# Performance work log

Measured on AMD Instinct MI355X. Metric: run time of the kernel, lower is better.

The kernel has to match this reference:

```python
import jax, jax.numpy as jnp
import numpy as np

N, F, H, E = 100000, 128, 128, 3200000
EPS = 1e-5


def setup_inputs() -> dict:
    key = jax.random.key(0)
    ks = jax.random.split(key, 16)
    g = lambda k, shape, fan_in: jax.random.normal(k, shape, jnp.float32) / np.sqrt(fan_in)
    inp = {
        'x': jax.random.normal(ks[0], (N, F), jnp.float32),
        'edge_index': jax.random.randint(ks[1], (2, E), 0, N, jnp.int64),
        # SAGEConv params: lin_l (aggregated-neighbor path, has bias), lin_r (root path, no bias)
        'W1l': g(ks[2], (F, H), F), 'b1': jnp.zeros((H,), jnp.float32), 'W1r': g(ks[3], (F, H), F),
        'W2l': g(ks[4], (H, H), H), 'b2': jnp.zeros((H,), jnp.float32), 'W2r': g(ks[5], (H, H), H),
        'W3l': g(ks[6], (H, H), H), 'b3': jnp.zeros((H,), jnp.float32), 'W3r': g(ks[7], (H, H), H),
        'W4l': g(ks[8], (H, 1), H), 'b4': jnp.zeros((1,), jnp.float32), 'W4r': g(ks[9], (H, 1), H),
        # BatchNorm affine params
        'g1': jnp.ones((H,), jnp.float32), 'be1': jnp.zeros((H,), jnp.float32),
        'g2': jnp.ones((H,), jnp.float32), 'be2': jnp.zeros((H,), jnp.float32),
        'g3': jnp.ones((H,), jnp.float32), 'be3': jnp.zeros((H,), jnp.float32),
        # shared residual linear
        'Wlin': g(ks[10], (H, H), H), 'blin': jnp.zeros((H,), jnp.float32),
    }
    return inp


def _sage(x, src, dst, Wl, b, Wr):
    # mean aggregation of source features at destination nodes
    n = x.shape[0]
    s = jax.ops.segment_sum(x[src], dst, num_segments=n)          # [N, d]
    cnt = jax.ops.segment_sum(jnp.ones_like(dst, x.dtype), dst, num_segments=n)
    agg = s / jnp.maximum(cnt, 1.0)[:, None]
    return agg @ Wl + b + x @ Wr


def _bn(x, gamma, beta):
    # training-mode batch norm over node dim (biased variance, as torch)
    mu = x.mean(0)
    var = jnp.mean((x - mu) ** 2, axis=0)
    return gamma * (x - mu) * jax.lax.rsqrt(var + EPS) + beta


def reference(x, edge_index, W1l, b1, W1r, W2l, b2, W2r, W3l, b3, W3r,
              W4l, b4, W4r, g1, be1, g2, be2, g3, be3, Wlin, blin):
    src, dst = edge_index[0], edge_index[1]
    # dropout is identity (eval-mode reference)
    x1 = jax.nn.elu(_bn(_sage(x, src, dst, W1l, b1, W1r), g1, be1))
    x2 = jax.nn.elu(_bn(_sage(x1, src, dst, W2l, b2, W2r), g2, be2))
    x2 = x2 + x1 @ Wlin + blin
    x3 = jax.nn.elu(_bn(_sage(x2, src, dst, W3l, b3, W3r), g3, be3))
    x3 = x3 + x2 @ Wlin + blin
    x4 = _sage(x3, src, dst, W4l, b4, W4r)  # [N, 1]
    return jnp.squeeze(x4, -1)
```

## Files before the change

kernel.cpp:

```cpp
#include <hip/hip_runtime.h>
#include <hip/hip_bf16.h>
#include <math.h>

#define BN_EPS 1e-5f

typedef __attribute__((ext_vector_type(8))) short bf16x8;
typedef __attribute__((ext_vector_type(4))) float f32x4;
typedef unsigned int uint32;

__device__ __forceinline__ unsigned bf16rne(float f) {
  unsigned u = __float_as_uint(f);
  unsigned r = u + 0x7fffu + ((u >> 16) & 1u);
  return r >> 16;
}
__device__ __forceinline__ float bf2f_lo(uint32 u) { return __uint_as_float(u << 16); }
__device__ __forceinline__ float bf2f_hi(uint32 u) { return __uint_as_float(u & 0xffff0000u); }
__device__ __forceinline__ uint32 packbf2(float a, float b) {
  return bf16rne(a) | (bf16rne(b) << 16);
}

__device__ __forceinline__ int edge_at(const int* __restrict__ ei, long long idx, int is64) {
  return is64 ? ei[2 * idx] : ei[idx];
}

__global__ void detect_kernel(const int* __restrict__ ei, long long E, int* __restrict__ flag) {
  __shared__ int found;
  int t = threadIdx.x;
  if (t == 0) found = 0;
  __syncthreads();
  long long npairs = E < 1024 ? E : 1024;
  for (long long p = t; p < npairs; p += blockDim.x)
    if (ei[2 * p + 1] != 0) found = 1;
  __syncthreads();
  if (t == 0) *flag = found ? 0 : 1;
}

__global__ void zero_i32_kernel(int* __restrict__ p, long long n) {
  long long i = blockIdx.x * (long long)blockDim.x + threadIdx.x;
  if (i < n) p[i] = 0;
}
__global__ void zero_f32_kernel(float* __restrict__ p, long long n) {
  long long i = blockIdx.x * (long long)blockDim.x + threadIdx.x;
  if (i < n) p[i] = 0.f;
}

__global__ void extract_count_kernel(const int* __restrict__ ei, long long E,
                                     const int* __restrict__ flag,
                                     int* __restrict__ es, int* __restrict__ r8,
                                     int* __restrict__ cnt8, int N) {
  long long e = blockIdx.x * (long long)blockDim.x + threadIdx.x;
  if (e >= E) return;
  int is64 = *flag;
  es[e] = edge_at(ei, e, is64);
  int d = edge_at(ei, E + e, is64);
  int sh = blockIdx.x & 7;
  r8[e] = atomicAdd(&cnt8[(size_t)sh * N + d], 1);
}

__global__ void cumnode_kernel(const int* __restrict__ cnt8, int* __restrict__ cum8,
                               int* __restrict__ cnt_node, int N) {
  int n = blockIdx.x * blockDim.x + threadIdx.x;
  if (n >= N) return;
  int run = 0;
#pragma unroll
  for (int sh = 0; sh < 8; ++sh) {
    int c = cnt8[(size_t)sh * N + n];
    cum8[(size_t)sh * N + n] = run;
    run += c;
  }
  cnt_node[n] = run;
}

__global__ void partial_kernel(const int* __restrict__ cnt, int* __restrict__ bsum, int M) {
  __shared__ int s[256];
  int b = blockIdx.x, t = threadIdx.x;
  int base = b * 2048 + t * 8;
  int sum = 0;
#pragma unroll
  for (int i = 0; i < 8; ++i) {
    int idx = base + i;
    if (idx < M) sum += cnt[idx];
  }
  s[t] = sum;
  __syncthreads();
  for (int d = 128; d > 0; d >>= 1) {
    if (t < d) s[t] += s[t + d];
    __syncthreads();
  }
  if (t == 0) bsum[b] = s[0];
}

__global__ void scanb_kernel(int* __restrict__ bsum, int nb) {
  __shared__ int s[512];
  int t = threadIdx.x;
  int v = (t < nb) ? bsum[t] : 0;
  s[t] = v;
  __syncthreads();
  for (int d = 1; d < 512; d <<= 1) {
    int u = (t >= d) ? s[t - d] : 0;
    __syncthreads();
    s[t] += u;
    __syncthreads();
  }
  if (t < nb) bsum[t] = s[t] - v;
}

__global__ void offsets_kernel(const int* __restrict__ cnt, const int* __restrict__ bsum,
                               int* __restrict__ off, int M, long long Etot) {
  __shared__ int s[256];
  int b = blockIdx.x, t = threadIdx.x;
  int base = b * 2048 + t * 8;
  int v[8];
  int sum = 0;
#pragma unroll
  for (int i = 0; i < 8; ++i) {
    int idx = base + i;
    v[i] = (idx < M) ? cnt[idx] : 0;
    sum += v[i];
  }
  s[t] = sum;
  __syncthreads();
  for (int d = 1; d < 256; d <<= 1) {
    int u = (t >= d) ? s[t - d] : 0;
    __syncthreads();
    s[t] += u;
    __syncthreads();
  }
  int run = bsum[b] + s[t] - sum;
#pragma unroll
  for (int i = 0; i < 8; ++i) {
    int idx = base + i;
    if (idx < M) {
      off[idx] = run;
      run += v[i];
    }
  }
  if (b == 0 && t == 0) off[M] = (int)Etot;
}

__global__ void pos_kernel(const int* __restrict__ ei, long long E, const int* __restrict__ flag,
                           const int* __restrict__ r8, const int* __restrict__ off_node,
                           const int* __restrict__ cum8, uint32* __restrict__ ppk, int N) {
  long long e = blockIdx.x * (long long)blockDim.x + threadIdx.x;
  if (e >= E) return;
  int is64 = *flag;
  int d = edge_at(ei, E + e, is64);
  int sh = blockIdx.x & 7;
  uint32 pos = (uint32)(off_node[d] + cum8[(size_t)sh * N + d] + r8[e]);
  uint32 region = (uint32)d >> 15;
  ppk[e] = pos | (region << 28);
}

__global__ void scatter_det_kernel(const int* __restrict__ es, const uint32* __restrict__ ppk,
                                   long long E, uint32 p, int* __restrict__ esrc) {
  long long e = blockIdx.x * (long long)blockDim.x + threadIdx.x;
  if (e >= E) return;
  uint32 v = ppk[e];
  if ((v >> 28) == p) esrc[v & 0x0FFFFFFFu] = es[e];
}

__global__ void convert_bf16_kernel(const float* __restrict__ x, uint32* __restrict__ xb,
                                    long long total2) {
  long long i = blockIdx.x * (long long)blockDim.x + threadIdx.x;
  if (i >= total2) return;
  float2 f = ((const float2*)x)[i];
  xb[i] = packbf2(f.x, f.y);
}

__global__ void repack_all_kernel(const float* __restrict__ Wa, const float* __restrict__ Wb,
                                  const float* __restrict__ Wc, const float* __restrict__ Wd,
                                  const float* __restrict__ We, const float* __restrict__ Wf,
                                  const float* __restrict__ Wg, ushort* __restrict__ Wp) {
  int wi = blockIdx.x >> 3;
  const float* W = wi == 0 ? Wa : wi == 1 ? Wb : wi == 2 ? Wc : wi == 3 ? Wd
                 : wi == 4 ? We : wi == 5 ? Wf : Wg;
  ushort* dst = Wp + (size_t)wi * 16384;
  int s = (blockIdx.x & 7) * 256 + threadIdx.x;
  int nt = s >> 8, rem = s & 255, ks = rem >> 6, lane = rem & 63;
  int q = lane >> 4, l16 = lane & 15;
  int kbase = ks * 32 + q * 8, c = nt * 16 + l16;
  uint32 out[4];
#pragma unroll
  for (int jp = 0; jp < 4; ++jp) {
    float a = W[(size_t)(kbase + 2 * jp) * 128 + c];
    float b = W[(size_t)(kbase + 2 * jp + 1) * 128 + c];
    out[jp] = packbf2(a, b);
  }
  ((uint4*)dst)[s] = make_uint4(out[0], out[1], out[2], out[3]);
}

__global__ void aggregate_bf16_kernel(const uint32* __restrict__ X, const int* __restrict__ off,
                                      const int* __restrict__ esrc, uint32* __restrict__ out,
                                      int N) {
  int gw = (int)((blockIdx.x * (long long)blockDim.x + threadIdx.x) >> 6);
  int lane = threadIdx.x & 63;
  if (gw >= N) return;
  int b = off[gw], e = off[gw + 1];
  int sub = lane & 15, grp = lane >> 4;
  const uint4* X4 = (const uint4*)X;
  float acc[8];
#pragma unroll
  for (int j = 0; j < 8; ++j) acc[j] = 0.f;
  for (int i = b; i < e; i += 8) {
    int i0 = i + grp, i1 = i + 4 + grp;
    bool h0 = i0 < e, h1 = i1 < e;
    uint4 v0 = make_uint4(0, 0, 0, 0), v1 = make_uint4(0, 0, 0, 0);
    if (h0) { int s0 = esrc[i0]; v0 = X4[(size_t)s0 * 16 + sub]; }
    if (h1) { int s1 = esrc[i1]; v1 = X4[(size_t)s1 * 16 + sub]; }
    if (h0) {
      acc[0] += bf2f_lo(v0.x); acc[1] += bf2f_hi(v0.x);
      acc[2] += bf2f_lo(v0.y); acc[3] += bf2f_hi(v0.y);
      acc[4] += bf2f_lo(v0.z); acc[5] += bf2f_hi(v0.z);
      acc[6] += bf2f_lo(v0.w); acc[7] += bf2f_hi(v0.w);
    }
    if (h1) {
      acc[0] += bf2f_lo(v1.x); acc[1] += bf2f_hi(v1.x);
      acc[2] += bf2f_lo(v1.y); acc[3] += bf2f_hi(v1.y);
      acc[4] += bf2f_lo(v1.z); acc[5] += bf2f_hi(v1.z);
      acc[6] += bf2f_lo(v1.w); acc[7] += bf2f_hi(v1.w);
    }
  }
#pragma unroll
  for (int j = 0; j < 8; ++j) {
    acc[j] += __shfl_xor(acc[j], 16, 64);
    acc[j] += __shfl_xor(acc[j], 32, 64);
  }
  if (grp == 0) {
    float inv = 1.0f / fmaxf((float)(e - b), 1.0f);
    uint4 o;
    o.x = packbf2(acc[0] * inv, acc[1] * inv);
    o.y = packbf2(acc[2] * inv, acc[3] * inv);
    o.z = packbf2(acc[4] * inv, acc[5] * inv);
    o.w = packbf2(acc[6] * inv, acc[7] * inv);
    ((uint4*)out)[(size_t)gw * 16 + sub] = o;
  }
}

__launch_bounds__(256)
__global__ void gemm_mfma_kernel(const ushort* __restrict__ A1, const ushort* __restrict__ W1p,
                                 const ushort* __restrict__ A2, const ushort* __restrict__ W2p,
                                 const ushort* __restrict__ W3p,
                                 const float* __restrict__ bias, const float* __restrict__ rbias,
                                 ushort* __restrict__ Y, ushort* __restrict__ R,
                                 float* __restrict__ bnsum, int N) {
  __shared__ float sred[16][128];
  int t = threadIdx.x;
  int w = t >> 6, lane = t & 63;
  int quad = lane >> 4, l16 = lane & 15;
  int row0 = blockIdx.x * 64 + w * 16;

  f32x4 accY[8], accR[8];
#pragma unroll
  for (int nt = 0; nt < 8; ++nt) {
    accY[nt][0] = accY[nt][1] = accY[nt][2] = accY[nt][3] = 0.f;
    accR[nt][0] = accR[nt][1] = accR[nt][2] = accR[nt][3] = 0.f;
  }

  int rowA = row0 + l16;
  if (rowA > N - 1) rowA = N - 1;
  const ushort* a1p = A1 + (size_t)rowA * 128 + quad * 8;
  const ushort* a2p = A2 + (size_t)rowA * 128 + quad * 8;
  const int haveR = (W3p != nullptr);

#pragma unroll
  for (int ks = 0; ks < 4; ++ks) {
    bf16x8 a = *(const bf16x8*)(a1p + ks * 32);
#pragma unroll
    for (int nt = 0; nt < 8; ++nt) {
      bf16x8 b = *(const bf16x8*)(W1p + ((size_t)(nt * 4 + ks) * 64 + lane) * 8);
      accY[nt] = __builtin_amdgcn_mfma_f32_16x16x32_bf16(a, b, accY[nt], 0, 0, 0);
    }
  }
#pragma unroll
  for (int ks = 0; ks < 4; ++ks) {
    bf16x8 a = *(const bf16x8*)(a2p + ks * 32);
#pragma unroll
    for (int nt = 0; nt < 8; ++nt) {
      bf16x8 b = *(const bf16x8*)(W2p + ((size_t)(nt * 4 + ks) * 64 + lane) * 8);
      accY[nt] = __builtin_amdgcn_mfma_f32_16x16x32_bf16(a, b, accY[nt], 0, 0, 0);
    }
    if (haveR) {
#pragma unroll
      for (int nt = 0; nt < 8; ++nt) {
        bf16x8 b = *(const bf16x8*)(W3p + ((size_t)(nt * 4 + ks) * 64 + lane) * 8);
        accR[nt] = __builtin_amdgcn_mfma_f32_16x16x32_bf16(a, b, accR[nt], 0, 0, 0);
      }
    }
  }

  float s1v[8], s2v[8];
#pragma unroll
  for (int nt = 0; nt < 8; ++nt) {
    int c = nt * 16 + l16;
    float bv = bias[c];
    s1v[nt] = 0.f; s2v[nt] = 0.f;
#pragma unroll
    for (int reg = 0; reg < 4; ++reg) {
      int grow = row0 + quad * 4 + reg;
      if (grow < N) {
        float v = accY[nt][reg] + bv;
        Y[(size_t)grow * 128 + c] = (ushort)bf16rne(v);
        s1v[nt] += v; s2v[nt] += v * v;
      }
    }
    if (haveR) {
      float rb = rbias[c];
#pragma unroll
      for (int reg = 0; reg < 4; ++reg) {
        int grow = row0 + quad * 4 + reg;
        if (grow < N) {
          float v = accR[nt][reg] + rb;
          R[(size_t)grow * 128 + c] = (ushort)bf16rne(v);
        }
      }
    }
  }

  int rrow = w * 4 + quad;
#pragma unroll
  for (int nt = 0; nt < 8; ++nt) sred[rrow][nt * 16 + l16] = s1v[nt];
  __syncthreads();
  if (t < 128) {
    float tot = 0.f;
#pragma unroll
    for (int r16 = 0; r16 < 16; ++r16) tot += sred[r16][t];
    atomicAdd(&bnsum[(size_t)(blockIdx.x & 63) * 256 + t], tot);
  }
  __syncthreads();
#pragma unroll
  for (int nt = 0; nt < 8; ++nt) sred[rrow][nt * 16 + l16] = s2v[nt];
  __syncthreads();
  if (t < 128) {
    float tot = 0.f;
#pragma unroll
    for (int r16 = 0; r16 < 16; ++r16) tot += sred[r16][t];
    atomicAdd(&bnsum[(size_t)(blockIdx.x & 63) * 256 + 128 + t], tot);
  }
}

__global__ void bn_finalize_kernel(const float* __restrict__ bnsum, float* __restrict__ bnp, int N) {
  int t = threadIdx.x;
  if (t < 128) {
    float s = 0.f, s2 = 0.f;
    for (int sh = 0; sh < 64; ++sh) {
      s  += bnsum[(size_t)sh * 256 + t];
      s2 += bnsum[(size_t)sh * 256 + 128 + t];
    }
    float invN = 1.0f / (float)N;
    float mu = s * invN;
    float var = s2 * invN - mu * mu;
    bnp[t] = mu;
    bnp[128 + t] = rsqrtf(var + BN_EPS);
  }
}

__global__ void bn_elu_kernel(const uint32* __restrict__ Y, const float* __restrict__ bnp,
                              const float* __restrict__ g, const float* __restrict__ be,
                              const uint32* __restrict__ res, uint32* __restrict__ Xo,
                              long long total2) {
  long long i = blockIdx.x * (long long)blockDim.x + threadIdx.x;
  if (i >= total2) return;
  int c0 = (int)(i & 63) * 2;
  uint32 y = Y[i];
  float v0 = g[c0]     * (bf2f_lo(y) - bnp[c0])     * bnp[128 + c0]     + be[c0];
  float v1 = g[c0 + 1] * (bf2f_hi(y) - bnp[c0 + 1]) * bnp[128 + c0 + 1] + be[c0 + 1];
  v0 = v0 > 0.f ? v0 : expm1f(v0);
  v1 = v1 > 0.f ? v1 : expm1f(v1);
  if (res) {
    uint32 rv = res[i];
    v0 += bf2f_lo(rv); v1 += bf2f_hi(rv);
  }
  Xo[i] = packbf2(v0, v1);
}

__global__ void dot4_kernel(const uint32* __restrict__ X, const float* __restrict__ W4l,
                            const float* __restrict__ W4r, float* __restrict__ z,
                            float* __restrict__ rr, int N) {
  int gw = (int)((blockIdx.x * (long long)blockDim.x + threadIdx.x) >> 6);
  int lane = threadIdx.x & 63;
  if (gw >= N) return;
  uint32 u = X[(size_t)gw * 64 + lane];
  float x0 = bf2f_lo(u), x1 = bf2f_hi(u);
  float wl0 = W4l[2 * lane], wl1 = W4l[2 * lane + 1];
  float wr0 = W4r[2 * lane], wr1 = W4r[2 * lane + 1];
  float a = x0 * wl0 + x1 * wl1;
  float b = x0 * wr0 + x1 * wr1;
  for (int d = 32; d > 0; d >>= 1) {
    a += __shfl_down(a, d, 64);
    b += __shfl_down(b, d, 64);
  }
  if (lane == 0) { z[gw] = a; rr[gw] = b; }
}

__global__ void final_kernel(const float* __restrict__ z, const float* __restrict__ rr,
                             const int* __restrict__ off, const int* __restrict__ esrc,
                             const float* __restrict__ b4, float* __restrict__ out, int N) {
  int n = blockIdx.x * blockDim.x + threadIdx.x;
  if (n >= N) return;
  int b = off[n], e = off[n + 1];
  float s = 0.f;
  for (int i = b; i < e; ++i) s += z[esrc[i]];
  out[n] = s / fmaxf((float)(e - b), 1.0f) + b4[0] + rr[n];
}

extern "C" void kernel_launch(void* const* d_in, const int* in_sizes, int n_in,
                              void* d_out, int out_size, void* d_ws, size_t ws_size,
                              hipStream_t stream) {
  const float* x   = (const float*)d_in[0];
  const int*   ei  = (const int*)d_in[1];
  const float* W1l = (const float*)d_in[2];
  const float* b1  = (const float*)d_in[3];
  const float* W1r = (const float*)d_in[4];
  const float* W2l = (const float*)d_in[5];
  const float* b2  = (const float*)d_in[6];
  const float* W2r = (const float*)d_in[7];
  const float* W3l = (const float*)d_in[8];
  const float* b3  = (const float*)d_in[9];
  const float* W3r = (const float*)d_in[10];
  const float* W4l = (const float*)d_in[11];
  const float* b4  = (const float*)d_in[12];
  const float* W4r = (const float*)d_in[13];
  const float* g1  = (const float*)d_in[14];
  const float* be1 = (const float*)d_in[15];
  const float* g2  = (const float*)d_in[16];
  const float* be2 = (const float*)d_in[17];
  const float* g3  = (const float*)d_in[18];
  const float* be3 = (const float*)d_in[19];
  const float* Wlin= (const float*)d_in[20];
  const float* blin= (const float*)d_in[21];

  const int N = in_sizes[0] / 128;
  const long long E = in_sizes[1] / 2;
  const int M = 8 * N;
  float* out = (float*)d_out;

  char* w = (char*)d_ws;
  size_t o = 0;
  auto alloc = [&](size_t bytes) -> char* {
    char* p = w + o;
    o = (o + bytes + 255) & ~(size_t)255;
    return p;
  };
  int*    off_node = (int*)alloc((size_t)(N + 1) * 4);
  int*    cnt_node = (int*)alloc((size_t)N * 4);
  int*    bsum     = (int*)alloc(512 * 4);
  int*    flag     = (int*)alloc(4);
  float*  bnsum    = (float*)alloc((size_t)64 * 256 * 4);
  float*  bnp      = (float*)alloc(256 * 4);
  float*  z        = (float*)alloc((size_t)N * 4);
  float*  rr       = (float*)alloc((size_t)N * 4);
  ushort* Wp       = (ushort*)alloc((size_t)7 * 2048 * 16);
  int*    esrc     = (int*)alloc((size_t)E * 4);
  size_t slotA = (size_t)2 * E * 4;
  size_t ysz = (size_t)N * 256;
  if (ysz > slotA) slotA = ysz;
  char* poolA  = alloc(slotA);
  char* poolB1 = alloc((size_t)N * 256);
  char* poolB3 = alloc((size_t)N * 256);
  uint32* B2   = (uint32*)alloc((size_t)N * 256);
  (void)ws_size; (void)n_in; (void)out_size;

  int*    es    = (int*)poolA;
  int*    r8    = (int*)(poolA + (size_t)E * 4);
  ushort* Ybuf  = (ushort*)poolA;
  int*    cnt8  = (int*)poolB1;
  int*    cum8  = cnt8 + M;
  uint32* ppk   = (uint32*)(cum8 + M);
  uint32* B1    = (uint32*)poolB1;
  uint32* B3    = (uint32*)poolB3;

  const int B = 256;
  const int eb  = (int)((E + B - 1) / B);
  const int nb  = (N + B - 1) / B;
  const int wb  = (int)(((long long)N * 64 + B - 1) / B);
  const int gb  = (N + 63) / 64;
  const long long tot2 = (long long)N * 64;
  const int cb  = (int)((tot2 + B - 1) / B);
  const int gN  = (N + 2047) / 2048;

  ushort* Wp1l = Wp + 0 * 16384;
  ushort* Wp1r = Wp + 1 * 16384;
  ushort* Wp2l = Wp + 2 * 16384;
  ushort* Wp2r = Wp + 3 * 16384;
  ushort* Wp3l = Wp + 4 * 16384;
  ushort* Wp3r = Wp + 5 * 16384;
  ushort* Wpln = Wp + 6 * 16384;

  detect_kernel<<<1, 1024, 0, stream>>>(ei, E, flag);
  zero_i32_kernel<<<(M + B - 1) / B, B, 0, stream>>>(cnt8, (long long)M);
  extract_count_kernel<<<eb, B, 0, stream>>>(ei, E, flag, es, r8, cnt8, N);
  cumnode_kernel<<<nb, B, 0, stream>>>(cnt8, cum8, cnt_node, N);
  partial_kernel<<<gN, B, 0, stream>>>(cnt_node, bsum, N);
  scanb_kernel<<<1, 512, 0, stream>>>(bsum, gN);
  offsets_kernel<<<gN, B, 0, stream>>>(cnt_node, bsum, off_node, N, E);
  pos_kernel<<<eb, B, 0, stream>>>(ei, E, flag, r8, off_node, cum8, ppk, N);
  for (uint32 p = 0; p < 4; ++p)
    scatter_det_kernel<<<eb, B, 0, stream>>>(es, ppk, E, p, esrc);

  convert_bf16_kernel<<<cb, B, 0, stream>>>(x, B1, tot2);
  repack_all_kernel<<<56, B, 0, stream>>>(W1l, W1r, W2l, W2r, W3l, W3r, Wlin, Wp);

  aggregate_bf16_kernel<<<wb, B, 0, stream>>>(B1, off_node, esrc, B2, N);
  zero_f32_kernel<<<64, B, 0, stream>>>(bnsum, 64 * 256);
  gemm_mfma_kernel<<<gb, B, 0, stream>>>((const ushort*)B2, Wp1l, (const ushort*)B1, Wp1r,
                                         nullptr, b1, nullptr, Ybuf, nullptr, bnsum, N);
  bn_finalize_kernel<<<1, 128, 0, stream>>>(bnsum, bnp, N);
  bn_elu_kernel<<<cb, B, 0, stream>>>((const uint32*)Ybuf, bnp, g1, be1, nullptr, B3, tot2);

  aggregate_bf16_kernel<<<wb, B, 0, stream>>>(B3, off_node, esrc, B2, N);
  zero_f32_kernel<<<64, B, 0, stream>>>(bnsum, 64 * 256);
  gemm_mfma_kernel<<<gb, B, 0, stream>>>((const ushort*)B2, Wp2l, (const ushort*)B3, Wp2r,
                                         Wpln, b2, blin, Ybuf, (ushort*)B1, bnsum, N);
  bn_finalize_kernel<<<1, 128, 0, stream>>>(bnsum, bnp, N);
  bn_elu_kernel<<<cb, B, 0, stream>>>((const uint32*)Ybuf, bnp, g2, be2, B1, B2, tot2);

  aggregate_bf16_kernel<<<wb, B, 0, stream>>>(B2, off_node, esrc, B3, N);
  zero_f32_kernel<<<64, B, 0, stream>>>(bnsum, 64 * 256);
  gemm_mfma_kernel<<<gb, B, 0, stream>>>((const ushort*)B3, Wp3l, (const ushort*)B2, Wp3r,
                                         Wpln, b3, blin, Ybuf, (ushort*)B1, bnsum, N);
  bn_finalize_kernel<<<1, 128, 0, stream>>>(bnsum, bnp, N);
  bn_elu_kernel<<<cb, B, 0, stream>>>((const uint32*)Ybuf, bnp, g3, be3, B1, B3, tot2);

  dot4_kernel<<<wb, B, 0, stream>>>(B3, W4l, W4r, z, rr, N);
  final_kernel<<<nb, B, 0, stream>>>(z, rr, off_node, esrc, b4, out, N);
}
```

Measured before the change: 992.5 us.

## Replace 8-way sharded edge counting with 64 per-block persistent histograms

Edge counting switches from 8 shards keyed by block index to 64 persistent blocks of 1024 threads, each with a private N-sized histogram. This spreads atomic contention across more copies and lets each block process a strided range of edges. A new fold kernel turns the histograms into absolute per-block offsets, so the position kernel needs only one lookup. The cost is a 64×N histogram (25.6 MB) that must be zeroed, summed and folded, plus only 64 blocks driving the edge loops, which may underuse the GPU.

```diff
diff --git a/kernel.cpp b/kernel.cpp
--- a/kernel.cpp
+++ b/kernel.cpp
@@ -3,6 +3,7 @@
 #include <math.h>
 
 #define BN_EPS 1e-5f
+#define GCNT 64
 
 typedef __attribute__((ext_vector_type(8))) short bf16x8;
 typedef __attribute__((ext_vector_type(4))) float f32x4;
@@ -47,28 +48,37 @@
 __global__ void extract_count_kernel(const int* __restrict__ ei, long long E,
                                      const int* __restrict__ flag,
                                      int* __restrict__ es, int* __restrict__ r8,
-                                     int* __restrict__ cnt8, int N) {
-  long long e = blockIdx.x * (long long)blockDim.x + threadIdx.x;
-  if (e >= E) return;
+                                     int* __restrict__ ghist, int N) {
+  int b = blockIdx.x;
   int is64 = *flag;
-  es[e] = edge_at(ei, e, is64);
-  int d = edge_at(ei, E + e, is64);
-  int sh = blockIdx.x & 7;
-  r8[e] = atomicAdd(&cnt8[(size_t)sh * N + d], 1);
-}
-
-__global__ void cumnode_kernel(const int* __restrict__ cnt8, int* __restrict__ cum8,
-                               int* __restrict__ cnt_node, int N) {
+  int* h = ghist + (size_t)b * N;
+  long long stride = (long long)GCNT * 1024;
+  for (long long e = (long long)b * 1024 + threadIdx.x; e < E; e += stride) {
+    es[e] = edge_at(ei, e, is64);
+    int d = edge_at(ei, E + e, is64);
+    r8[e] = atomicAdd(&h[d], 1);
+  }
+}
+
+__global__ void sum64_kernel(const int* __restrict__ ghist, int* __restrict__ cnt_node, int N) {
   int n = blockIdx.x * blockDim.x + threadIdx.x;
   if (n >= N) return;
-  int run = 0;
-#pragma unroll
-  for (int sh = 0; sh < 8; ++sh) {
-    int c = cnt8[(size_t)sh * N + n];
-    cum8[(size_t)sh * N + n] = run;
-    run += c;
-  }
-  cnt_node[n] = run;
+  int s = 0;
+#pragma unroll 8
+  for (int b = 0; b < GCNT; ++b) s += ghist[(size_t)b * N + n];
+  cnt_node[n] = s;
+}
+
+__global__ void fold_kernel(int* __restrict__ ghist, const int* __restrict__ off_node, int N) {
+  int n = blockIdx.x * blockDim.x + threadIdx.x;
+  if (n >= N) return;
+  int run = off_node[n];
+  for (int b = 0; b < GCNT; ++b) {
+    size_t idx = (size_t)b * N + n;
+    int t = ghist[idx];
+    ghist[idx] = run;
+    run += t;
+  }
 }
 
 __global__ void partial_kernel(const int* __restrict__ cnt, int* __restrict__ bsum, int M) {
@@ -139,16 +149,18 @@
 }
 
 __global__ void pos_kernel(const int* __restrict__ ei, long long E, const int* __restrict__ flag,
-                           const int* __restrict__ r8, const int* __restrict__ off_node,
-                           const int* __restrict__ cum8, uint32* __restrict__ ppk, int N) {
-  long long e = blockIdx.x * (long long)blockDim.x + threadIdx.x;
-  if (e >= E) return;
+                           const int* __restrict__ r8, const int* __restrict__ ghist,
+                           uint32* __restrict__ ppk, int N) {
+  int b = blockIdx.x;
   int is64 = *flag;
-  int d = edge_at(ei, E + e, is64);
-  int sh = blockIdx.x & 7;
-  uint32 pos = (uint32)(off_node[d] + cum8[(size_t)sh * N + d] + r8[e]);
-  uint32 region = (uint32)d >> 15;
-  ppk[e] = pos | (region << 28);
+  const int* h = ghist + (size_t)b * N;
+  long long stride = (long long)GCNT * 1024;
+  for (long long e = (long long)b * 1024 + threadIdx.x; e < E; e += stride) {
+    int d = edge_at(ei, E + e, is64);
+    uint32 pos = (uint32)(h[d] + r8[e]);
+    uint32 region = (uint32)d >> 15;
+    ppk[e] = pos | (region << 28);
+  }
 }
 
 __global__ void scatter_det_kernel(const int* __restrict__ es, const uint32* __restrict__ ppk,
@@ -431,7 +443,6 @@
 
   const int N = in_sizes[0] / 128;
   const long long E = in_sizes[1] / 2;
-  const int M = 8 * N;
   float* out = (float*)d_out;
 
   char* w = (char*)d_ws;
@@ -463,10 +474,9 @@
   int*    es    = (int*)poolA;
   int*    r8    = (int*)(poolA + (size_t)E * 4);
   ushort* Ybuf  = (ushort*)poolA;
-  int*    cnt8  = (int*)poolB1;
-  int*    cum8  = cnt8 + M;
-  uint32* ppk   = (uint32*)(cum8 + M);
+  int*    ghist = (int*)poolB1;
   uint32* B1    = (uint32*)poolB1;
+  uint32* ppk   = (uint32*)poolB3;
   uint32* B3    = (uint32*)poolB3;
 
   const int B = 256;
@@ -477,6 +487,7 @@
   const long long tot2 = (long long)N * 64;
   const int cb  = (int)((tot2 + B - 1) / B);
   const int gN  = (N + 2047) / 2048;
+  const long long ghn = (long long)GCNT * N;
 
   ushort* Wp1l = Wp + 0 * 16384;
   ushort* Wp1r = Wp + 1 * 16384;
@@ -487,13 +498,14 @@
   ushort* Wpln = Wp + 6 * 16384;
 
   detect_kernel<<<1, 1024, 0, stream>>>(ei, E, flag);
-  zero_i32_kernel<<<(M + B - 1) / B, B, 0, stream>>>(cnt8, (long long)M);
-  extract_count_kernel<<<eb, B, 0, stream>>>(ei, E, flag, es, r8, cnt8, N);
-  cumnode_kernel<<<nb, B, 0, stream>>>(cnt8, cum8, cnt_node, N);
+  zero_i32_kernel<<<(int)((ghn + B - 1) / B), B, 0, stream>>>(ghist, ghn);
+  extract_count_kernel<<<GCNT, 1024, 0, stream>>>(ei, E, flag, es, r8, ghist, N);
+  sum64_kernel<<<nb, B, 0, stream>>>(ghist, cnt_node, N);
   partial_kernel<<<gN, B, 0, stream>>>(cnt_node, bsum, N);
   scanb_kernel<<<1, 512, 0, stream>>>(bsum, gN);
   offsets_kernel<<<gN, B, 0, stream>>>(cnt_node, bsum, off_node, N, E);
-  pos_kernel<<<eb, B, 0, stream>>>(ei, E, flag, r8, off_node, cum8, ppk, N);
+  fold_kernel<<<nb, B, 0, stream>>>(ghist, off_node, N);
+  pos_kernel<<<GCNT, 1024, 0, stream>>>(ei, E, flag, r8, ghist, ppk, N);
   for (uint32 p = 0; p < 4; ++p)
     scatter_det_kernel<<<eb, B, 0, stream>>>(es, ppk, E, p, esrc);
 
```

New measurement: 1.090 ms. 9.8% more time.
